# Kernel optimization log

Hardware: AMD Instinct MI355X
Metric: run time of the kernel (lower is better)

## Reference

```python
import jax, jax.numpy as jnp
import numpy as np

L_K = 6  # number of nearest neighbors (matches module-level L_K)
N_POINTS = 4096


def setup_inputs() -> dict:
    key = jax.random.key(0)
    k1, k2, k3, k4 = jax.random.split(key, 4)
    input_t = jax.random.normal(k1, (1, 3, N_POINTS), dtype=jnp.float32)
    sf_t = jax.random.normal(k2, (1, 3, N_POINTS), dtype=jnp.float32) * 0.1
    y1 = jax.random.normal(k3, (1, 3, N_POINTS), dtype=jnp.float32)
    pred = jax.random.normal(k4, (1, 3, N_POINTS), dtype=jnp.float32)
    return {"input_t": input_t, "sf_t": sf_t, "y1": y1, "pred": pred}


def _kabsch(pc, recon):
    # Standard Kabsch rigid-transform estimation (pc, recon: [N,3]).
    cp = pc.mean(axis=0)
    cr = recon.mean(axis=0)
    H = (pc - cp).T @ (recon - cr)  # [3,3] cross-covariance
    U, S, Vt = jnp.linalg.svd(H)
    d = jnp.sign(jnp.linalg.det(Vt.T @ U.T))
    # R = V diag(1,1,d) U^T  (reflection fix)
    R = Vt.T @ (jnp.stack([jnp.float32(1.0), jnp.float32(1.0), d])[:, None] * U.T)
    t = cr - R @ cp
    return R, t


def _knn_laplace(centers, ref, k):
    # centers: [N,3] query points (x1); ref: [M,3] cloud to gather neighbors from.
    # Matches: squared_dist over all pairs, topk smallest along ref dim,
    # grouping gather, then Laplacian differencing normalized by (k-1).
    d2 = jnp.sum((centers[:, None, :] - ref[None, :, :]) ** 2, axis=-1)  # [N,M]
    _, idx = jax.lax.top_k(-d2, k)  # k smallest distances -> neighbor indices [N,k]
    grouped = ref[idx]  # [N,k,3] gather
    return jnp.sum(grouped - centers[:, None, :], axis=1) / float(k - 1)  # [N,3]


def reference(input_t, sf_t, y1, pred):
    # Rigid reconstruction: we use a single cluster covering all points
    # (deterministic stand-in for the CPU-side DBSCAN clustering), so the
    # whole cloud is rigidly reconstructed via Kabsch, then detached
    # (original code calls .detach() on the Kabsch reconstruction).
    pc = input_t[0].T        # [N,3]
    recon = pc + sf_t[0].T   # [N,3]
    R, t = _kabsch(pc, recon)
    rigid_recon = jax.lax.stop_gradient(pc @ R.T + t)  # [N,3]

    yT = y1[0].T  # [N,3]
    laplace_y = _knn_laplace(rigid_recon, yT, L_K)          # cross-cloud kNN Laplacian
    laplace_x = _knn_laplace(rigid_recon, rigid_recon, L_K)  # self kNN Laplacian
    laplace_reduced = laplace_x - laplace_y  # [N,3]

    # Single cluster = all points: subtract mean Laplacian difference.
    rigid_refine = rigid_recon - jnp.mean(laplace_reduced, axis=0)  # [N,3]

    # L1 loss (mean reduction) vs student prediction.
    return jnp.mean(jnp.abs(rigid_refine - pred[0].T))
```

## Files before the change

kernel.cpp:

```cpp
#include <hip/hip_runtime.h>
#include <math.h>

#define NP 4096
#define KNN 6
#define NCHUNK 16
#define CHUNK 256

typedef unsigned int u32;
typedef unsigned long long u64;

__device__ inline double wave_reduce(double v) {
#pragma unroll
  for (int o = 32; o > 0; o >>= 1) v += __shfl_down(v, o);
  return v;
}

__device__ inline float det3f(const float M[3][3]) {
  return M[0][0]*(M[1][1]*M[2][2]-M[1][2]*M[2][1])
       - M[0][1]*(M[1][0]*M[2][2]-M[1][2]*M[2][0])
       + M[0][2]*(M[1][0]*M[2][1]-M[1][1]*M[2][0]);
}

#define TOP6_INSERT_ILP(key)                                          \
  { u32 m0 = max(b0, key), m1 = max(b1, key), m2 = max(b2, key),      \
        m3 = max(b3, key), m4 = max(b4, key);                         \
    b0 = min(b0, key); b1 = min(b1, m0); b2 = min(b2, m1);            \
    b3 = min(b3, m2); b4 = min(b4, m3); b5 = min(b5, m4); }

__global__ __launch_bounds__(256) void k1_kabsch_pack(const float* __restrict__ in,
                                                      const float* __restrict__ sf,
                                                      const float* __restrict__ ycloud,
                                                      float4* __restrict__ cand0,
                                                      float4* __restrict__ cand1,
                                                      u32* __restrict__ counter) {
  const int tid = threadIdx.x;
  const int lane = tid & 63, wv = tid >> 6;
  double acc[15];
#pragma unroll
  for (int q = 0; q < 15; ++q) acc[q] = 0.0;
  for (int i = tid; i < NP; i += 256) {
    double px = in[i], py = in[NP + i], pz = in[2*NP + i];
    double qx = px + (double)sf[i];
    double qy = py + (double)sf[NP + i];
    double qz = pz + (double)sf[2*NP + i];
    acc[0] += px; acc[1] += py; acc[2] += pz;
    acc[3] += qx; acc[4] += qy; acc[5] += qz;
    acc[6] += px*qx; acc[7]  += px*qy; acc[8]  += px*qz;
    acc[9] += py*qx; acc[10] += py*qy; acc[11] += py*qz;
    acc[12]+= pz*qx; acc[13] += pz*qy; acc[14] += pz*qz;
  }
  __shared__ double wred[4][15];
#pragma unroll
  for (int q = 0; q < 15; ++q) {
    double v = wave_reduce(acc[q]);
    if (lane == 0) wred[wv][q] = v;
  }
  __syncthreads();
  __shared__ float Rts[12];
  if (tid == 0) {
    double tot[15];
    for (int q = 0; q < 15; ++q)
      tot[q] = wred[0][q] + wred[1][q] + wred[2][q] + wred[3][q];
    const double invN = 1.0 / (double)NP;
    double cp[3] = { tot[0]*invN, tot[1]*invN, tot[2]*invN };
    double cr[3] = { tot[3]*invN, tot[4]*invN, tot[5]*invN };
    float H[3][3];
    for (int a = 0; a < 3; ++a)
      for (int b = 0; b < 3; ++b)
        H[a][b] = (float)(tot[6 + a*3 + b] - (double)NP * cp[a] * cr[b]);
    float A[3][3];
    for (int a = 0; a < 3; ++a)
      for (int b = 0; b < 3; ++b)
        A[a][b] = H[0][a]*H[0][b] + H[1][a]*H[1][b] + H[2][a]*H[2][b];
    float V[3][3] = {{1,0,0},{0,1,0},{0,0,1}};
    const int PQ[3][2] = {{0,1},{0,2},{1,2}};
    for (int sweep = 0; sweep < 8; ++sweep) {
      for (int r = 0; r < 3; ++r) {
        const int p = PQ[r][0], q = PQ[r][1];
        float apq = A[p][q];
        if (fabsf(apq) > 1e-30f) {
          float theta = (A[q][q] - A[p][p]) / (2.0f * apq);
          float tt = copysignf(1.0f, theta) / (fabsf(theta) + sqrtf(theta*theta + 1.0f));
          float c = 1.0f / sqrtf(tt*tt + 1.0f);
          float s = tt * c;
          for (int k = 0; k < 3; ++k) { float akp=A[k][p], akq=A[k][q]; A[k][p]=c*akp - s*akq; A[k][q]=s*akp + c*akq; }
          for (int k = 0; k < 3; ++k) { float apk=A[p][k], aqk=A[q][k]; A[p][k]=c*apk - s*aqk; A[q][k]=s*apk + c*aqk; }
          for (int k = 0; k < 3; ++k) { float vkp=V[k][p], vkq=V[k][q]; V[k][p]=c*vkp - s*vkq; V[k][q]=s*vkp + c*vkq; }
        }
      }
    }
    int ord[3] = {0,1,2};
    for (int a = 0; a < 2; ++a)
      for (int b = a + 1; b < 3; ++b)
        if (A[ord[b]][ord[b]] > A[ord[a]][ord[a]]) { int t2 = ord[a]; ord[a] = ord[b]; ord[b] = t2; }
    float Vc[3][3], Uc[3][3];
    for (int j = 0; j < 3; ++j) {
      const int e = ord[j];
      float lam = A[e][e] > 0.0f ? A[e][e] : 0.0f;
      float sv = sqrtf(lam);
      float isv = sv > 1e-20f ? 1.0f / sv : 0.0f;
      for (int a = 0; a < 3; ++a) Vc[a][j] = V[a][e];
      for (int a = 0; a < 3; ++a)
        Uc[a][j] = (H[a][0]*Vc[0][j] + H[a][1]*Vc[1][j] + H[a][2]*Vc[2][j]) * isv;
    }
    float dd = (det3f(Uc) * det3f(Vc)) >= 0.0f ? 1.0f : -1.0f;
    float R[3][3];
    for (int a = 0; a < 3; ++a)
      for (int b = 0; b < 3; ++b)
        R[a][b] = Vc[a][0]*Uc[b][0] + Vc[a][1]*Uc[b][1] + dd * Vc[a][2]*Uc[b][2];
    for (int a = 0; a < 3; ++a) {
      Rts[a*3+0] = R[a][0]; Rts[a*3+1] = R[a][1]; Rts[a*3+2] = R[a][2];
      Rts[9+a] = (float)(cr[a] - ((double)R[a][0]*cp[0] + (double)R[a][1]*cp[1]
                                  + (double)R[a][2]*cp[2]));
    }
    *counter = 0u;
  }
  __syncthreads();
  const float r0=Rts[0], r1=Rts[1], r2=Rts[2];
  const float r3=Rts[3], r4=Rts[4], r5=Rts[5];
  const float r6=Rts[6], r7=Rts[7], r8=Rts[8];
  const float t0=Rts[9], t1=Rts[10], t2=Rts[11];
  for (int i = tid; i < NP; i += 256) {
    float px = in[i], py = in[NP + i], pz = in[2*NP + i];
    float a = fmaf(r0, px, fmaf(r1, py, fmaf(r2, pz, t0)));
    float b = fmaf(r3, px, fmaf(r4, py, fmaf(r5, pz, t1)));
    float c = fmaf(r6, px, fmaf(r7, py, fmaf(r8, pz, t2)));
    cand0[i] = make_float4(a, b, c, fmaf(a, a, fmaf(b, b, c * c)));
    float yx = ycloud[i], yy = ycloud[NP + i], yz = ycloud[2*NP + i];
    cand1[i] = make_float4(yx, yy, yz, fmaf(yx, yx, fmaf(yy, yy, yz * yz)));
  }
}

__global__ __launch_bounds__(256) void k2_scan(const float4* __restrict__ cand0,
                                               const float4* __restrict__ cand1,
                                               u32* __restrict__ part) {
  const int tid = threadIdx.x;
  const int chunk = blockIdx.x, cblk = blockIdx.y, cloud = blockIdx.z;
  const int j0 = chunk * CHUNK;
  const float4* __restrict__ cand = cloud ? cand1 : cand0;
  const int ci = cblk * CHUNK + tid;
  const float4 ct = cand0[ci];
  const float ax = -2.f*ct.x, ay = -2.f*ct.y, az = -2.f*ct.z;
  u32 b0=~0u, b1=~0u, b2=~0u, b3=~0u, b4=~0u, b5=~0u;
#pragma unroll 8
  for (int j = 0; j < CHUNK; ++j) {
    float4 c = cand[j0 + j];
    float s = fmaf(c.x, ax, fmaf(c.y, ay, fmaf(c.z, az, c.w)));
    u32 bits = __float_as_uint(s);
    u32 u = bits ^ ((u32)((int)bits >> 31) | 0x80000000u);
    u32 key = (u & 0xFFFFF000u) | (u32)(j0 + j);
    TOP6_INSERT_ILP(key);
  }
  u32* o = part + (size_t)(cloud * NCHUNK + chunk) * KNN * NP + ci;
  o[0*NP] = b0; o[1*NP] = b1; o[2*NP] = b2;
  o[3*NP] = b3; o[4*NP] = b4; o[5*NP] = b5;
}

__global__ __launch_bounds__(256) void k3_merge_final(const u32* __restrict__ part,
                                                      const float4* __restrict__ cand0,
                                                      const float4* __restrict__ cand1,
                                                      const float* __restrict__ pred,
                                                      double* __restrict__ blockpart,
                                                      u32* __restrict__ counter,
                                                      float* __restrict__ out) {
  const int tid = threadIdx.x;
  const int lane = tid & 63, wv = tid >> 6;
  const int cloud = blockIdx.x >> 4, cblk = blockIdx.x & 15;
  const int ci = cblk * 256 + tid;
  u32 b0=~0u, b1=~0u, b2=~0u, b3=~0u, b4=~0u, b5=~0u;
  for (int c = 0; c < NCHUNK; ++c) {
    const u32* p = part + (size_t)(cloud * NCHUNK + c) * KNN * NP + ci;
#pragma unroll
    for (int e = 0; e < KNN; ++e) {
      u32 key = p[(size_t)e * NP];
      TOP6_INSERT_ILP(key);
    }
  }
  u32 bk[KNN] = { b0, b1, b2, b3, b4, b5 };
  const float4* __restrict__ g = cloud ? cand1 : cand0;
  float s0 = 0.f, s1 = 0.f, s2 = 0.f;
#pragma unroll
  for (int k = 0; k < KNN; ++k) {
    float4 nb = g[bk[k] & 0xFFFu];
    s0 += nb.x; s1 += nb.y; s2 += nb.z;
  }
  const double sgn = cloud ? -1.0 : 1.0;
  double v0 = wave_reduce(sgn * (double)s0);
  double v1 = wave_reduce(sgn * (double)s1);
  double v2 = wave_reduce(sgn * (double)s2);
  __shared__ double wred[4][3];
  __shared__ int lastFlag;
  if (lane == 0) { wred[wv][0] = v0; wred[wv][1] = v1; wred[wv][2] = v2; }
  __syncthreads();
  if (tid == 0) {
    for (int q = 0; q < 3; ++q) {
      double B = wred[0][q] + wred[1][q] + wred[2][q] + wred[3][q];
      atomicExch((u64*)&blockpart[blockIdx.x * 3 + q], (u64)__double_as_longlong(B));
    }
    __threadfence();
    u32 t = atomicAdd(counter, 1u);
    lastFlag = (t == 31u);
  }
  __syncthreads();
  if (!lastFlag) return;

  __shared__ double bp[96];
  __threadfence();
  if (tid < 96)
    bp[tid] = __longlong_as_double((long long)atomicAdd((u64*)&blockpart[tid], 0ULL));
  __syncthreads();
  __shared__ float m[3];
  if (tid == 0) {
    double a0 = 0.0, a1 = 0.0, a2 = 0.0;
    for (int b = 0; b < 32; ++b) {
      a0 += bp[b*3 + 0]; a1 += bp[b*3 + 1]; a2 += bp[b*3 + 2];
    }
    const double sc = 0.2 / (double)NP;
    m[0] = (float)(a0 * sc); m[1] = (float)(a1 * sc); m[2] = (float)(a2 * sc);
  }
  __syncthreads();
  const float m0 = m[0], m1 = m[1], m2 = m[2];
  double s = 0.0;
  for (int i = tid; i < NP; i += 256) {
    float4 rc = cand0[i];
    s += (double)fabsf(rc.x - m0 - pred[i]);
    s += (double)fabsf(rc.y - m1 - pred[NP + i]);
    s += (double)fabsf(rc.z - m2 - pred[2*NP + i]);
  }
  double v = wave_reduce(s);
  __shared__ double fred[4];
  if (lane == 0) fred[wv] = v;
  __syncthreads();
  if (tid == 0)
    out[0] = (float)((fred[0] + fred[1] + fred[2] + fred[3]) / (3.0 * (double)NP));
}

extern "C" void kernel_launch(void* const* d_in, const int* in_sizes, int n_in,
                              void* d_out, int out_size, void* d_ws, size_t ws_size,
                              hipStream_t stream) {
  const float* in   = (const float*)d_in[0];
  const float* sf   = (const float*)d_in[1];
  const float* y1   = (const float*)d_in[2];
  const float* pred = (const float*)d_in[3];

  u32* part = (u32*)d_ws;
  double* blockpart = (double*)(part + (size_t)2*NCHUNK*KNN*NP);
  u32* counter = (u32*)(blockpart + 96);
  float4* cand0 = (float4*)(counter + 4);
  float4* cand1 = cand0 + NP;

  k1_kabsch_pack<<<1, 256, 0, stream>>>(in, sf, y1, cand0, cand1, counter);
  k2_scan<<<dim3(NCHUNK, 16, 2), 256, 0, stream>>>(cand0, cand1, part);
  k3_merge_final<<<32, 256, 0, stream>>>(part, cand0, cand1, pred,
                                         blockpart, counter, (float*)d_out);
}
```

Before: 64.28 us.

## Stage candidate chunk in LDS and compute two queries per thread in kNN scan

```diff
diff --git a/kernel.cpp b/kernel.cpp
--- a/kernel.cpp
+++ b/kernel.cpp
@@ -3,8 +3,8 @@
 
 #define NP 4096
 #define KNN 6
-#define NCHUNK 16
-#define CHUNK 256
+#define NCH 32
+#define CHUNK 128
 
 typedef unsigned int u32;
 typedef unsigned long long u64;
@@ -21,7 +21,7 @@
        + M[0][2]*(M[1][0]*M[2][1]-M[1][1]*M[2][0]);
 }
 
-#define TOP6_INSERT_ILP(key)                                          \
+#define TOP6_INS(b0,b1,b2,b3,b4,b5,key)                               \
   { u32 m0 = max(b0, key), m1 = max(b1, key), m2 = max(b2, key),      \
         m3 = max(b3, key), m4 = max(b4, key);                         \
     b0 = min(b0, key); b1 = min(b1, m0); b2 = min(b2, m1);            \
@@ -134,26 +134,37 @@
 __global__ __launch_bounds__(256) void k2_scan(const float4* __restrict__ cand0,
                                                const float4* __restrict__ cand1,
                                                u32* __restrict__ part) {
+  __shared__ float4 sc[CHUNK];
   const int tid = threadIdx.x;
   const int chunk = blockIdx.x, cblk = blockIdx.y, cloud = blockIdx.z;
   const int j0 = chunk * CHUNK;
   const float4* __restrict__ cand = cloud ? cand1 : cand0;
-  const int ci = cblk * CHUNK + tid;
-  const float4 ct = cand0[ci];
-  const float ax = -2.f*ct.x, ay = -2.f*ct.y, az = -2.f*ct.z;
-  u32 b0=~0u, b1=~0u, b2=~0u, b3=~0u, b4=~0u, b5=~0u;
+  if (tid < CHUNK) sc[tid] = cand[j0 + tid];
+  const int ci0 = cblk * 512 + tid;
+  const int ci1 = ci0 + 256;
+  const float4 ctA = cand0[ci0];
+  const float4 ctB = cand0[ci1];
+  const float axA = -2.f*ctA.x, ayA = -2.f*ctA.y, azA = -2.f*ctA.z, wA = ctA.w;
+  const float axB = -2.f*ctB.x, ayB = -2.f*ctB.y, azB = -2.f*ctB.z, wB = ctB.w;
+  __syncthreads();
+  u32 a0=~0u,a1=~0u,a2=~0u,a3=~0u,a4=~0u,a5=~0u;
+  u32 c0=~0u,c1=~0u,c2=~0u,c3=~0u,c4=~0u,c5=~0u;
 #pragma unroll 8
   for (int j = 0; j < CHUNK; ++j) {
-    float4 c = cand[j0 + j];
-    float s = fmaf(c.x, ax, fmaf(c.y, ay, fmaf(c.z, az, c.w)));
-    u32 bits = __float_as_uint(s);
-    u32 u = bits ^ ((u32)((int)bits >> 31) | 0x80000000u);
-    u32 key = (u & 0xFFFFF000u) | (u32)(j0 + j);
-    TOP6_INSERT_ILP(key);
-  }
-  u32* o = part + (size_t)(cloud * NCHUNK + chunk) * KNN * NP + ci;
-  o[0*NP] = b0; o[1*NP] = b1; o[2*NP] = b2;
-  o[3*NP] = b3; o[4*NP] = b4; o[5*NP] = b5;
+    float4 c = sc[j];
+    float sA = fmaf(c.x, axA, fmaf(c.y, ayA, fmaf(c.z, azA, c.w))) + wA;
+    float sB = fmaf(c.x, axB, fmaf(c.y, ayB, fmaf(c.z, azB, c.w))) + wB;
+    sA = fmaxf(sA, 0.f);
+    sB = fmaxf(sB, 0.f);
+    u32 kA = (__float_as_uint(sA) & 0xFFFFF000u) | (u32)(j0 + j);
+    u32 kB = (__float_as_uint(sB) & 0xFFFFF000u) | (u32)(j0 + j);
+    TOP6_INS(a0,a1,a2,a3,a4,a5,kA);
+    TOP6_INS(c0,c1,c2,c3,c4,c5,kB);
+  }
+  u32* oA = part + (size_t)(cloud * NCH + chunk) * KNN * NP + ci0;
+  oA[0*NP]=a0; oA[1*NP]=a1; oA[2*NP]=a2; oA[3*NP]=a3; oA[4*NP]=a4; oA[5*NP]=a5;
+  u32* oB = part + (size_t)(cloud * NCH + chunk) * KNN * NP + ci1;
+  oB[0*NP]=c0; oB[1*NP]=c1; oB[2*NP]=c2; oB[3*NP]=c3; oB[4*NP]=c4; oB[5*NP]=c5;
 }
 
 __global__ __launch_bounds__(256) void k3_merge_final(const u32* __restrict__ part,
@@ -168,12 +179,12 @@
   const int cloud = blockIdx.x >> 4, cblk = blockIdx.x & 15;
   const int ci = cblk * 256 + tid;
   u32 b0=~0u, b1=~0u, b2=~0u, b3=~0u, b4=~0u, b5=~0u;
-  for (int c = 0; c < NCHUNK; ++c) {
-    const u32* p = part + (size_t)(cloud * NCHUNK + c) * KNN * NP + ci;
+  for (int c = 0; c < NCH; ++c) {
+    const u32* p = part + (size_t)(cloud * NCH + c) * KNN * NP + ci;
 #pragma unroll
     for (int e = 0; e < KNN; ++e) {
       u32 key = p[(size_t)e * NP];
-      TOP6_INSERT_ILP(key);
+      TOP6_INS(b0,b1,b2,b3,b4,b5,key);
     }
   }
   u32 bk[KNN] = { b0, b1, b2, b3, b4, b5 };
@@ -211,12 +222,12 @@
   __syncthreads();
   __shared__ float m[3];
   if (tid == 0) {
-    double a0 = 0.0, a1 = 0.0, a2 = 0.0;
+    double q0 = 0.0, q1 = 0.0, q2 = 0.0;
     for (int b = 0; b < 32; ++b) {
-      a0 += bp[b*3 + 0]; a1 += bp[b*3 + 1]; a2 += bp[b*3 + 2];
+      q0 += bp[b*3 + 0]; q1 += bp[b*3 + 1]; q2 += bp[b*3 + 2];
     }
     const double sc = 0.2 / (double)NP;
-    m[0] = (float)(a0 * sc); m[1] = (float)(a1 * sc); m[2] = (float)(a2 * sc);
+    m[0] = (float)(q0 * sc); m[1] = (float)(q1 * sc); m[2] = (float)(q2 * sc);
   }
   __syncthreads();
   const float m0 = m[0], m1 = m[1], m2 = m[2];
@@ -244,13 +255,13 @@
   const float* pred = (const float*)d_in[3];
 
   u32* part = (u32*)d_ws;
-  double* blockpart = (double*)(part + (size_t)2*NCHUNK*KNN*NP);
+  double* blockpart = (double*)(part + (size_t)2*NCH*KNN*NP);
   u32* counter = (u32*)(blockpart + 96);
   float4* cand0 = (float4*)(counter + 4);
   float4* cand1 = cand0 + NP;
 
   k1_kabsch_pack<<<1, 256, 0, stream>>>(in, sf, y1, cand0, cand1, counter);
-  k2_scan<<<dim3(NCHUNK, 16, 2), 256, 0, stream>>>(cand0, cand1, part);
+  k2_scan<<<dim3(NCH, 8, 2), 256, 0, stream>>>(cand0, cand1, part);
   k3_merge_final<<<32, 256, 0, stream>>>(part, cand0, cand1, pred,
                                          blockpart, counter, (float*)d_out);
 }
```

Measured after the change: 66.55 us. 3.5% more time.
